# Kernel tuning notes

Measured on AMD Instinct MI355X. Metric: run time of the kernel, lower is better.

The kernel has to match this reference:

```python
import jax, jax.numpy as jnp
import numpy as np

N = 50000
E = 800000
G_DIM = 512
H1 = 128
H2 = 128
R = 8  # 2 * n_speakers**2


def setup_inputs() -> dict:
    key = jax.random.key(0)
    ks = jax.random.split(key, 16)
    s = lambda d: 1.0 / np.sqrt(d)
    inp = {
        'node_features': jax.random.normal(ks[0], (N, G_DIM), jnp.float32),
        'edge_index': jax.random.randint(ks[1], (2, E), 0, N, jnp.int64),
        'edge_type': jax.random.randint(ks[2], (E,), 0, R, jnp.int64),
        # RGCNConv params
        'W_rel': jax.random.normal(ks[3], (R, G_DIM, H1), jnp.float32) * s(G_DIM),
        'W_root': jax.random.normal(ks[4], (G_DIM, H1), jnp.float32) * s(G_DIM),
        'b1': jnp.zeros((H1,), jnp.float32),
        # TransformerConv params (heads=1)
        'Wq': jax.random.normal(ks[5], (H1, H2), jnp.float32) * s(H1),
        'bq': jnp.zeros((H2,), jnp.float32),
        'Wk': jax.random.normal(ks[6], (H1, H2), jnp.float32) * s(H1),
        'bk': jnp.zeros((H2,), jnp.float32),
        'Wv': jax.random.normal(ks[7], (H1, H2), jnp.float32) * s(H1),
        'bv': jnp.zeros((H2,), jnp.float32),
        'Wskip': jax.random.normal(ks[8], (H1, H2), jnp.float32) * s(H1),
        'bskip': jnp.zeros((H2,), jnp.float32),
        # BatchNorm1d params
        'gamma': jnp.ones((H2,), jnp.float32),
        'beta': jnp.zeros((H2,), jnp.float32),
    }
    return inp


def reference(node_features, edge_index, edge_type, W_rel, W_root, b1,
              Wq, bq, Wk, bk, Wv, bv, Wskip, bskip, gamma, beta):
    n = node_features.shape[0]
    r = W_rel.shape[0]
    src, dst = edge_index[0], edge_index[1]

    # ---- RGCNConv: per-relation mean aggregation + root + bias ----
    # x @ W_r for all relations, then per-edge gather: [n,r,h1] -> [E,h1]
    xW = jnp.einsum('nf,rfh->nrh', node_features, W_rel)
    msg = xW[src, edge_type]                         # [E, H1]
    comp = dst * r + edge_type                       # composite (node, relation) key
    cnt = jax.ops.segment_sum(jnp.ones((msg.shape[0],), msg.dtype), comp,
                              num_segments=n * r)
    denom = jnp.maximum(cnt[comp], 1.0)[:, None]     # mean within each (node, rel)
    agg1 = jax.ops.segment_sum(msg / denom, dst, num_segments=n)
    h = agg1 + node_features @ W_root + b1           # [n, H1]

    # ---- TransformerConv (heads=1): segment-softmax attention ----
    q = h @ Wq + bq
    k = h @ Wk + bk
    v = h @ Wv + bv
    d = q.shape[-1]
    score = jnp.sum(q[dst] * k[src], axis=-1) / jnp.sqrt(jnp.float32(d))  # [E]
    smax = jax.ops.segment_max(score, dst, num_segments=n)
    smax = jnp.where(jnp.isfinite(smax), smax, 0.0)
    ex = jnp.exp(score - smax[dst])
    ssum = jax.ops.segment_sum(ex, dst, num_segments=n)
    alpha = ex / jnp.maximum(ssum[dst], 1e-16)       # [E]
    agg2 = jax.ops.segment_sum(alpha[:, None] * v[src], dst, num_segments=n)
    h2 = agg2 + h @ Wskip + bskip                    # root (lin_skip) path

    # ---- BatchNorm1d (training mode: batch stats) + LeakyReLU(0.01) ----
    mu = jnp.mean(h2, axis=0)
    var = jnp.mean((h2 - mu) ** 2, axis=0)
    xn = (h2 - mu) / jnp.sqrt(var + 1e-5)
    out = gamma * xn + beta
    return jnp.where(out >= 0, out, 0.01 * out)
```

## Files before the change

kernel.cpp:

```cpp
#include <hip/hip_runtime.h>

typedef float f32x4 __attribute__((ext_vector_type(4)));
typedef _Float16 f16x8 __attribute__((ext_vector_type(8)));
typedef _Float16 f16x2 __attribute__((ext_vector_type(2)));

#define NN 50000
#define EE 800000
#define GD 512
#define H1C 128
#define RR 8
#define NC1 1152
#define NC2 512
#define NCAST (NN * GD / 4)
#define PREPN (NCAST + NC1 * GD + NC2 * H1C)

__device__ __forceinline__ unsigned short f2h(float f){
  _Float16 h = (_Float16)f;
  unsigned short u; __builtin_memcpy(&u, &h, 2); return u;
}
__device__ __forceinline__ float h2f(unsigned short u){
  _Float16 h; __builtin_memcpy(&h, &u, 2); return (float)h;
}
__device__ __forceinline__ void gload16(const void* g, void* l){
  __builtin_amdgcn_global_load_lds(
      (const __attribute__((address_space(1))) unsigned int*)g,
      (__attribute__((address_space(3))) unsigned int*)l, 16, 0, 0);
}
__device__ __forceinline__ float dot2(f16x2 a, f16x2 b, float c){
#if __has_builtin(__builtin_amdgcn_fdot2)
  return __builtin_amdgcn_fdot2(a, b, c, false);
#else
  return c + (float)a[0] * (float)b[0] + (float)a[1] * (float)b[1];
#endif
}

__global__ void k_zero(unsigned* __restrict__ zp, int n){
  int i = blockIdx.x * 256 + threadIdx.x;
  if (i < n) zp[i] = 0u;
}

__global__ void k_prep(const float* __restrict__ x, unsigned short* __restrict__ x16,
                       const float* __restrict__ W_rel, const float* __restrict__ W_root,
                       unsigned short* __restrict__ wcatT,
                       const float* __restrict__ Wq, const float* __restrict__ Wk,
                       const float* __restrict__ Wv, const float* __restrict__ Ws,
                       const float* __restrict__ bq, const float* __restrict__ bk,
                       const float* __restrict__ bv, const float* __restrict__ bs,
                       unsigned short* __restrict__ w2T, float* __restrict__ bias2,
                       const int* __restrict__ ei, const int* __restrict__ et,
                       float* __restrict__ cnt){
  int i = blockIdx.x * 256 + threadIdx.x;
  if (i >= PREPN){
    int e = i - PREPN;
    if (e < EE) atomicAdd(&cnt[(size_t)ei[EE + e] * RR + et[e]], 1.0f);
    return;
  }
  if (i < NCAST){
    int b = i * 4;
    float4 v = *(const float4*)(x + b);
    ushort4 o;
    o.x = f2h(v.x); o.y = f2h(v.y); o.z = f2h(v.z); o.w = f2h(v.w);
    *(ushort4*)(x16 + b) = o;
    return;
  }
  i -= NCAST;
  if (i < NC1 * GD){
    int j = i >> 9;
    int f = i & 511;
    float v;
    if (j < 1024) v = W_rel[((size_t)(j >> 7) * GD + f) * H1C + (j & 127)];
    else          v = W_root[(size_t)f * H1C + (j - 1024)];
    wcatT[(size_t)j * GD + f] = f2h(v);
    return;
  }
  i -= NC1 * GD;
  if (i < NC2 * H1C){
    int j = i >> 7;
    int f = i & 127;
    int m = j >> 7;
    int hc = j & 127;
    const float* W = (m == 0) ? Wq : (m == 1) ? Wk : (m == 2) ? Wv : Ws;
    w2T[(size_t)j * H1C + f] = f2h(W[(size_t)f * H1C + hc]);
    if (f == 0){
      const float* B = (m == 0) ? bq : (m == 1) ? bk : (m == 2) ? bv : bs;
      bias2[j] = B[hc];
    }
  }
}

__global__ void k_alloc(const float* __restrict__ cnt, int* __restrict__ deg,
                        int* __restrict__ basea, int* __restrict__ cur,
                        unsigned* __restrict__ total, int n){
  int v = blockIdx.x * 256 + threadIdx.x;
  if (v >= n) return;
  const float4* c = (const float4*)(cnt + (size_t)v * 8);
  float4 a = c[0], b = c[1];
  int d = (int)(a.x + a.y + a.z + a.w + b.x + b.y + b.z + b.w + 0.5f);
  deg[v] = d;
  int base = (int)atomicAdd(total, (unsigned)d);
  basea[v] = base;
  cur[v] = base;
}

__global__ void k_scatter_perm(const int* __restrict__ ei, const int* __restrict__ et,
                               int* __restrict__ cur, unsigned* __restrict__ sortedSR, int E){
  int e = blockIdx.x * blockDim.x + threadIdx.x;
  if (e >= E) return;
  int dst = ei[E + e];
  int pos = atomicAdd(&cur[dst], 1);
  sortedSR[pos] = (unsigned)(ei[e] & 0xFFFF) | ((unsigned)et[e] << 16);
}

#define TILE 128
#define BK 64

__global__ __launch_bounds__(256) void k_gemm(
    const unsigned short* __restrict__ A,
    const unsigned short* __restrict__ Bt,
    unsigned short* __restrict__ C,
    const float* __restrict__ bias,
    int M, int Nout, int K, int rowsPerXcd, int colBlocks)
{
  int bid = blockIdx.x;
  int xcd = bid & 7;
  int lin = bid >> 3;
  int rowb = xcd * rowsPerXcd + lin / colBlocks;
  int colb = lin % colBlocks;
  int row0 = rowb * TILE;
  if (row0 >= M) return;
  int col0 = colb * TILE;

  __shared__ unsigned short As[TILE][BK];
  __shared__ unsigned short Bs[TILE][BK];
  int tid = threadIdx.x;
  int wave = tid >> 6, lane = tid & 63;
  int wm = (wave >> 1) * 64, wn = (wave & 1) * 64;
  int l16 = lane & 15, quad = lane >> 4;

  int srow = lane >> 3;
  int gcb  = ((lane & 7) ^ srow) * 8;
  int xorr = l16 & 7;

  f32x4 acc[4][4] = {};

  for (int k0 = 0; k0 < K; k0 += BK){
    __syncthreads();
    #pragma unroll
    for (int i = 0; i < 4; i++){
      int rbase = (wave * 4 + i) * 8;
      int gr = row0 + rbase + srow; if (gr >= M) gr = M - 1;
      gload16(A + (size_t)gr * K + k0 + gcb, &As[rbase][0]);
    }
    #pragma unroll
    for (int i = 0; i < 4; i++){
      int rbase = (wave * 4 + i) * 8;
      int gc = col0 + rbase + srow;
      gload16(Bt + (size_t)gc * K + k0 + gcb, &Bs[rbase][0]);
    }
    __syncthreads();
    #pragma unroll
    for (int ks = 0; ks < BK; ks += 32){
      int scol = ((quad + (ks >> 3)) ^ xorr) * 8;
      f16x8 af[4], bfr[4];
      #pragma unroll
      for (int i = 0; i < 4; i++) af[i] = *(const f16x8*)&As[wm + i*16 + l16][scol];
      #pragma unroll
      for (int j = 0; j < 4; j++) bfr[j] = *(const f16x8*)&Bs[wn + j*16 + l16][scol];
      #pragma unroll
      for (int i = 0; i < 4; i++)
        #pragma unroll
        for (int j = 0; j < 4; j++)
          acc[i][j] = __builtin_amdgcn_mfma_f32_16x16x32_f16(af[i], bfr[j], acc[i][j], 0, 0, 0);
    }
  }

  #pragma unroll
  for (int i = 0; i < 4; i++){
    int rbase = row0 + wm + i*16 + quad*4;
    #pragma unroll
    for (int j = 0; j < 4; j++){
      int col = col0 + wn + j*16 + l16;
      float b = bias ? bias[col] : 0.0f;
      #pragma unroll
      for (int rr = 0; rr < 4; rr++){
        int row = rbase + rr;
        if (row < M) C[(size_t)row * Nout + col] = f2h(acc[i][j][rr] + b);
      }
    }
  }
}

__global__ __launch_bounds__(256) void k_rgcn_seg(
    const int* __restrict__ base, const int* __restrict__ deg,
    const unsigned* __restrict__ srt,
    const unsigned short* __restrict__ xW, const float* __restrict__ cnt,
    const float* __restrict__ b1, unsigned short* __restrict__ h16)
{
  int v = blockIdx.x * 4 + (threadIdx.x >> 6);
  if (v >= NN) return;
  int lane = threadIdx.x & 63;
  int g = lane >> 4, l16 = lane & 15;
  int start = base[v], d = deg[v];
  const float* cv = cnt + (size_t)v * RR;

  float o[8] = {};
  for (int cb = 0; cb < d; cb += 16){
    int srcs[4]; int rels[4]; float invs[4];
    #pragma unroll
    for (int t = 0; t < 4; t++){
      int idx = cb + 4 * t + g;
      bool valid = idx < d;
      unsigned sri = valid ? srt[start + idx] : 0u;
      srcs[t] = (int)(sri & 0xFFFFu);
      rels[t] = (int)(sri >> 16);
      invs[t] = valid ? 1.0f / fmaxf(cv[rels[t]], 1.0f) : 0.0f;
    }
    uint4 u[4];
    #pragma unroll
    for (int t = 0; t < 4; t++)
      u[t] = *(const uint4*)(xW + (size_t)srcs[t] * NC1 + rels[t] * H1C + l16 * 8);
    #pragma unroll
    for (int t = 0; t < 4; t++){
      const unsigned short* p = (const unsigned short*)&u[t];
      #pragma unroll
      for (int j = 0; j < 8; j++) o[j] += h2f(p[j]) * invs[t];
    }
  }
  #pragma unroll
  for (int j = 0; j < 8; j++){
    o[j] += __shfl_xor(o[j], 16, 64);
    o[j] += __shfl_xor(o[j], 32, 64);
  }
  if (g == 0){
    uint4 r = *(const uint4*)(xW + (size_t)v * NC1 + 1024 + l16 * 8);
    const unsigned short* p = (const unsigned short*)&r;
    unsigned short res[8];
    #pragma unroll
    for (int j = 0; j < 8; j++) res[j] = f2h(o[j] + h2f(p[j]) + b1[l16 * 8 + j]);
    *(uint4*)(h16 + (size_t)v * H1C + l16 * 8) = *(uint4*)res;
  }
}

__global__ __launch_bounds__(256) void k_attn3(
    const int* __restrict__ base, const int* __restrict__ deg,
    const unsigned* __restrict__ srt,
    const unsigned short* __restrict__ qkvs, float* __restrict__ h2)
{
  int v = blockIdx.x * 4 + (threadIdx.x >> 6);
  if (v >= NN) return;
  int lane = threadIdx.x & 63;
  int g = lane >> 4, l16 = lane & 15;
  int start = base[v], d = deg[v];
  const float sc = 0.08838834764831845f;

  uint4 qa = *(const uint4*)(qkvs + (size_t)v * NC2 + l16 * 8);
  const f16x2* qh = (const f16x2*)&qa;

  float o[8] = {};
  float m = -INFINITY, l = 0.0f;

  for (int cb = 0; cb < d; cb += 16){
    int srcs[4]; bool val[4];
    #pragma unroll
    for (int t = 0; t < 4; t++){
      int idx = cb + 4 * t + g;
      val[t] = idx < d;
      srcs[t] = val[t] ? (int)(srt[start + idx] & 0xFFFFu) : 0;
    }
    uint4 ka[4], va[4];
    #pragma unroll
    for (int t = 0; t < 4; t++)
      ka[t] = *(const uint4*)(qkvs + (size_t)srcs[t] * NC2 + 128 + l16 * 8);
    #pragma unroll
    for (int t = 0; t < 4; t++)
      va[t] = *(const uint4*)(qkvs + (size_t)srcs[t] * NC2 + 256 + l16 * 8);

    float s[4];
    #pragma unroll
    for (int t = 0; t < 4; t++){
      const f16x2* kh = (const f16x2*)&ka[t];
      float ss = 0.0f;
      #pragma unroll
      for (int i = 0; i < 4; i++) ss = dot2(qh[i], kh[i], ss);
      #pragma unroll
      for (int off = 8; off >= 1; off >>= 1) ss += __shfl_xor(ss, off, 16);
      s[t] = val[t] ? ss * sc : -INFINITY;
    }

    float m4 = fmaxf(fmaxf(s[0], s[1]), fmaxf(s[2], s[3]));
    m4 = fmaxf(m4, __shfl_xor(m4, 16, 64));
    m4 = fmaxf(m4, __shfl_xor(m4, 32, 64));
    float newm = fmaxf(m, m4);
    float scale = __expf(m - newm);
    float e[4], esum = 0.0f;
    #pragma unroll
    for (int t = 0; t < 4; t++){
      e[t] = val[t] ? __expf(s[t] - newm) : 0.0f;
      esum += e[t];
    }
    esum += __shfl_xor(esum, 16, 64);
    esum += __shfl_xor(esum, 32, 64);
    l = l * scale + esum;

    #pragma unroll
    for (int j = 0; j < 8; j++) o[j] *= scale;
    #pragma unroll
    for (int t = 0; t < 4; t++){
      const unsigned short* p = (const unsigned short*)&va[t];
      #pragma unroll
      for (int j = 0; j < 8; j++) o[j] += e[t] * h2f(p[j]);
    }
    m = newm;
  }

  #pragma unroll
  for (int j = 0; j < 8; j++){
    o[j] += __shfl_xor(o[j], 16, 64);
    o[j] += __shfl_xor(o[j], 32, 64);
  }
  if (g == 0){
    float r = (d > 0) ? 1.0f / fmaxf(l, 1e-16f) : 0.0f;
    uint4 sk = *(const uint4*)(qkvs + (size_t)v * NC2 + 384 + l16 * 8);
    const unsigned short* p = (const unsigned short*)&sk;
    float* hd = h2 + (size_t)v * H1C + l16 * 8;
    float4 r0 = make_float4(h2f(p[0]) + o[0]*r, h2f(p[1]) + o[1]*r,
                            h2f(p[2]) + o[2]*r, h2f(p[3]) + o[3]*r);
    float4 r1 = make_float4(h2f(p[4]) + o[4]*r, h2f(p[5]) + o[5]*r,
                            h2f(p[6]) + o[6]*r, h2f(p[7]) + o[7]*r);
    *(float4*)hd = r0;
    *(float4*)(hd + 4) = r1;
  }
}

__global__ __launch_bounds__(256) void k_bn_reduce(const float* __restrict__ h2,
                                                   float* __restrict__ bn, int Nrows){
  __shared__ float ls[256], lq[256];
  int c = threadIdx.x & 127;
  int half = threadIdx.x >> 7;
  float s = 0.0f, q = 0.0f;
  for (int r = blockIdx.x * 2 + half; r < Nrows; r += gridDim.x * 2){
    float v = h2[(size_t)r * H1C + c];
    s += v; q += v * v;
  }
  ls[threadIdx.x] = s; lq[threadIdx.x] = q;
  __syncthreads();
  if (half == 0){
    atomicAdd(&bn[c],        ls[c] + ls[c + 128]);
    atomicAdd(&bn[128 + c],  lq[c] + lq[c + 128]);
  }
}

__global__ void k_out(const float* __restrict__ h2, const float* __restrict__ bn,
                      const float* __restrict__ gamma, const float* __restrict__ beta,
                      float* __restrict__ out, int n, float invN){
  int idx = blockIdx.x * blockDim.x + threadIdx.x;
  if (idx >= n) return;
  int c = idx & 127;
  float mu = bn[c] * invN;
  float var = bn[128 + c] * invN - mu * mu;
  float rs = rsqrtf(var + 1e-5f);
  float v = (h2[idx] - mu) * rs;
  float o = gamma[c] * v + beta[c];
  out[idx] = (o >= 0.0f) ? o : 0.01f * o;
}

extern "C" void kernel_launch(void* const* d_in, const int* in_sizes, int n_in,
                              void* d_out, int out_size, void* d_ws, size_t ws_size,
                              hipStream_t stream) {
  const float* x      = (const float*)d_in[0];
  const int*   ei     = (const int*)d_in[1];
  const int*   et     = (const int*)d_in[2];
  const float* W_rel  = (const float*)d_in[3];
  const float* W_root = (const float*)d_in[4];
  const float* b1     = (const float*)d_in[5];
  const float* Wq     = (const float*)d_in[6];
  const float* bq     = (const float*)d_in[7];
  const float* Wk     = (const float*)d_in[8];
  const float* bk     = (const float*)d_in[9];
  const float* Wv     = (const float*)d_in[10];
  const float* bv     = (const float*)d_in[11];
  const float* Wskip  = (const float*)d_in[12];
  const float* bskip  = (const float*)d_in[13];
  const float* gamma  = (const float*)d_in[14];
  const float* beta   = (const float*)d_in[15];
  float* out = (float*)d_out;

  const int N = NN, E = EE;
  char* ws = (char*)d_ws;
  size_t off = 0;
  auto alloc = [&](size_t bytes){ size_t r = off; off = (off + bytes + 255) & ~(size_t)255; return r; };

  size_t o_x16   = alloc((size_t)N * GD * 2);
  size_t o_w1    = alloc((size_t)NC1 * GD * 2);
  size_t o_xw    = alloc((size_t)N * NC1 * 2);
  size_t o_cnt   = alloc((size_t)N * RR * 4);
  size_t o_bn    = alloc((size_t)512 * 4);
  size_t o_tot   = alloc((size_t)64 * 4);
  size_t o_zend  = off;
  size_t o_deg   = alloc((size_t)N * 4);
  size_t o_base  = alloc((size_t)N * 4);
  size_t o_cur   = alloc((size_t)N * 4);
  size_t o_srt   = alloc((size_t)E * 4);
  size_t o_h16   = alloc((size_t)N * H1C * 2);
  size_t o_w2    = alloc((size_t)NC2 * H1C * 2);
  size_t o_b2    = alloc((size_t)NC2 * 4);

  unsigned short* x16   = (unsigned short*)(ws + o_x16);
  unsigned short* qkvs  = (unsigned short*)(ws + o_x16);
  unsigned short* wcatT = (unsigned short*)(ws + o_w1);
  unsigned short* xW    = (unsigned short*)(ws + o_xw);
  float*          h2    = (float*)(ws + o_xw);
  float*          cnt   = (float*)(ws + o_cnt);
  float*          bn    = (float*)(ws + o_bn);
  unsigned*       total = (unsigned*)(ws + o_tot);
  int*            deg   = (int*)(ws + o_deg);
  int*            basea = (int*)(ws + o_base);
  int*            cur   = (int*)(ws + o_cur);
  unsigned*       srt   = (unsigned*)(ws + o_srt);
  unsigned short* h16   = (unsigned short*)(ws + o_h16);
  unsigned short* w2T   = (unsigned short*)(ws + o_w2);
  float*          bias2 = (float*)(ws + o_b2);

  const int TPB = 256;
  const int ROWB = (N + TILE - 1) / TILE;
  const int RPX  = (ROWB + 7) / 8;
  const int HISTB = (E + TPB - 1) / TPB;

  int nzero = (int)((o_zend - o_cnt) / 4);
  k_zero<<<(nzero + TPB - 1) / TPB, TPB, 0, stream>>>((unsigned*)(ws + o_cnt), nzero);

  k_prep<<<PREPN / TPB + HISTB, TPB, 0, stream>>>(
      x, x16, W_rel, W_root, wcatT,
      Wq, Wk, Wv, Wskip, bq, bk, bv, bskip, w2T, bias2,
      ei, et, cnt);

  k_gemm<<<8 * RPX * (NC1 / TILE), TPB, 0, stream>>>(x16, wcatT, xW, nullptr,
      N, NC1, GD, RPX, NC1 / TILE);

  k_alloc<<<(N + TPB - 1) / TPB, TPB, 0, stream>>>(cnt, deg, basea, cur, total, N);
  k_scatter_perm<<<HISTB, TPB, 0, stream>>>(ei, et, cur, srt, E);

  k_rgcn_seg<<<(N + 3) / 4, TPB, 0, stream>>>(basea, deg, srt, xW, cnt, b1, h16);

  k_gemm<<<8 * RPX * (NC2 / TILE), TPB, 0, stream>>>(h16, w2T, qkvs, bias2,
      N, NC2, H1C, RPX, NC2 / TILE);

  k_attn3<<<(N + 3) / 4, TPB, 0, stream>>>(basea, deg, srt, qkvs, h2);

  k_bn_reduce<<<256, TPB, 0, stream>>>(h2, bn, N);
  k_out<<<((size_t)N * H1C + TPB - 1) / TPB, TPB, 0, stream>>>(h2, bn, gamma, beta, out, N * H1C, 1.0f / N);
}
```

Baseline: 567.6 us.

## Double-buffer GEMM LDS tiles with async global-to-LDS prefetch

Converts the fp16 MFMA GEMM main loop to a two-stage LDS ping-pong. The next K-tile's global_load_lds is issued while the current tile is consumed, with explicit vmcnt waits and sched barriers. This is meant to hide global load latency behind MFMA work. It doubles LDS use per block, which may lower occupancy, and relies on hand-placed waitcnt and barrier ordering to stay correct.

```diff
diff --git a/kernel.cpp b/kernel.cpp
--- a/kernel.cpp
+++ b/kernel.cpp
@@ -33,6 +33,11 @@
   return c + (float)a[0] * (float)b[0] + (float)a[1] * (float)b[1];
 #endif
 }
+
+#define SCHED0() __builtin_amdgcn_sched_barrier(0)
+#define WAITVM8() do { asm volatile("s_waitcnt vmcnt(8)" ::: "memory"); SCHED0(); } while(0)
+#define WAITVM0() do { asm volatile("s_waitcnt vmcnt(0)" ::: "memory"); SCHED0(); } while(0)
+#define BARRIER() do { SCHED0(); __builtin_amdgcn_s_barrier(); SCHED0(); } while(0)
 
 __global__ void k_zero(unsigned* __restrict__ zp, int n){
   int i = blockIdx.x * 256 + threadIdx.x;
@@ -130,8 +135,8 @@
   if (row0 >= M) return;
   int col0 = colb * TILE;
 
-  __shared__ unsigned short As[TILE][BK];
-  __shared__ unsigned short Bs[TILE][BK];
+  __shared__ unsigned short As[2][TILE][BK];
+  __shared__ unsigned short Bs[2][TILE][BK];
   int tid = threadIdx.x;
   int wave = tid >> 6, lane = tid & 63;
   int wm = (wave >> 1) * 64, wn = (wave & 1) * 64;
@@ -143,35 +148,47 @@
 
   f32x4 acc[4][4] = {};
 
-  for (int k0 = 0; k0 < K; k0 += BK){
-    __syncthreads();
+  auto stage = [&](int b, int k0){
     #pragma unroll
     for (int i = 0; i < 4; i++){
       int rbase = (wave * 4 + i) * 8;
       int gr = row0 + rbase + srow; if (gr >= M) gr = M - 1;
-      gload16(A + (size_t)gr * K + k0 + gcb, &As[rbase][0]);
+      gload16(A + (size_t)gr * K + k0 + gcb, &As[b][rbase][0]);
     }
     #pragma unroll
     for (int i = 0; i < 4; i++){
       int rbase = (wave * 4 + i) * 8;
       int gc = col0 + rbase + srow;
-      gload16(Bt + (size_t)gc * K + k0 + gcb, &Bs[rbase][0]);
-    }
-    __syncthreads();
+      gload16(Bt + (size_t)gc * K + k0 + gcb, &Bs[b][rbase][0]);
+    }
+  };
+
+  const int nk = K / BK;
+  stage(0, 0);
+  if (nk > 1) stage(1, BK);
+  SCHED0();
+
+  int cur = 0;
+  for (int t = 0; t < nk; ++t){
+    if (t < nk - 1) { WAITVM8(); } else { WAITVM0(); }
+    BARRIER();
     #pragma unroll
     for (int ks = 0; ks < BK; ks += 32){
       int scol = ((quad + (ks >> 3)) ^ xorr) * 8;
       f16x8 af[4], bfr[4];
       #pragma unroll
-      for (int i = 0; i < 4; i++) af[i] = *(const f16x8*)&As[wm + i*16 + l16][scol];
-      #pragma unroll
-      for (int j = 0; j < 4; j++) bfr[j] = *(const f16x8*)&Bs[wn + j*16 + l16][scol];
+      for (int i = 0; i < 4; i++) af[i] = *(const f16x8*)&As[cur][wm + i*16 + l16][scol];
+      #pragma unroll
+      for (int j = 0; j < 4; j++) bfr[j] = *(const f16x8*)&Bs[cur][wn + j*16 + l16][scol];
       #pragma unroll
       for (int i = 0; i < 4; i++)
         #pragma unroll
         for (int j = 0; j < 4; j++)
           acc[i][j] = __builtin_amdgcn_mfma_f32_16x16x32_f16(af[i], bfr[j], acc[i][j], 0, 0, 0);
     }
+    BARRIER();
+    if (t + 2 < nk) stage(cur, (t + 2) * BK);
+    cur ^= 1;
   }
 
   #pragma unroll
```

Result: slower. 601.8 us (+6.0%).
